# Kernel optimization log

Hardware: AMD Instinct MI355X
Metric: run time of the kernel (lower is better)

The kernel has to match this reference:

```python
import jax, jax.numpy as jnp
import numpy as np

N = 10000      # nodes
E = 320000     # edges (avg degree 32)
D_IN, D_H, D_OUT = 128, 256, 64


def setup_inputs() -> dict:
    key = jax.random.key(0)
    k0, k1, k2, k3 = jax.random.split(key, 4)
    x = jax.random.normal(k0, (N, D_IN), dtype=jnp.float32)
    edge_index = jax.random.randint(k1, (2, E), 0, N, dtype=jnp.int64)
    W1 = jax.random.normal(k2, (D_IN, D_H), dtype=jnp.float32) * 0.05
    b1 = jnp.zeros((D_H,), dtype=jnp.float32)
    W2 = jax.random.normal(k3, (D_H, D_OUT), dtype=jnp.float32) * 0.05
    b2 = jnp.zeros((D_OUT,), dtype=jnp.float32)
    return {"x": x, "edge_index": edge_index, "W1": W1, "b1": b1, "W2": W2, "b2": b2}


def gcn_conv(x, src, dst, W, b, n):
    """PyG GCNConv: linear transform, add self-loops, symmetric D^-1/2 (A+I) D^-1/2 aggregation."""
    h = x @ W                                               # [n, d_out]
    ones = jnp.ones(src.shape[0], dtype=h.dtype)
    deg = jax.ops.segment_sum(ones, dst, num_segments=n) + 1.0  # +1 for self-loop
    dinv = jax.lax.rsqrt(deg)                               # deg^{-1/2}
    norm = (dinv[src] * dinv[dst])[:, None]                 # per-edge coefficient
    agg = jax.ops.segment_sum(h[src] * norm, dst, num_segments=n)
    agg = agg + h * (1.0 / deg)[:, None]                    # self-loop: deg_i^{-1/2}*deg_i^{-1/2}
    return agg + b


def reference(x, edge_index, W1, b1, W2, b2):
    src, dst = edge_index[0], edge_index[1]
    h = jax.nn.relu(gcn_conv(x, src, dst, W1, b1, N))
    z = gcn_conv(h, src, dst, W2, b2, N)                    # [N, D_OUT]
    # decode: pairwise euclidean distance (torch.cdist p=2)
    sq = jnp.sum(z * z, axis=1)                             # [N]
    d2 = sq[:, None] + sq[None, :] - 2.0 * (z @ z.T)        # [N, N]
    d2 = jnp.maximum(d2, 0.0)
    pos = d2 > 0
    dist = jnp.where(pos, jnp.sqrt(jnp.where(pos, d2, 1.0)), 0.0)
    m = jnp.max(dist)
    m = jnp.where(m == 0, jnp.ones((), dist.dtype), m)
    return 1.0 - dist / m
```

## Files before the change

### kernel.cpp

```cpp
#include <hip/hip_runtime.h>
#include <hip/hip_bf16.h>
#include <cstdint>
#include <cstddef>

#define D_IN  128
#define D_H   256
#define D_OUT 64

typedef __attribute__((ext_vector_type(4))) float f32x4;
typedef __attribute__((ext_vector_type(8))) short s16x8;

__device__ __forceinline__ unsigned short f2bf(float f) {
  unsigned u = __float_as_uint(f);
  return (unsigned short)((u + 0x7fffu + ((u >> 16) & 1u)) >> 16);
}
__device__ __forceinline__ float bf2f(unsigned short b) {
  return __uint_as_float(((unsigned)b) << 16);
}

__global__ void prep_k(const int* __restrict__ raw, int* __restrict__ cnt,
                       int* __restrict__ cursor, int* __restrict__ gmax,
                       unsigned short* __restrict__ zb, int* __restrict__ src,
                       int* __restrict__ dst, int n, int npadElems, int E) {
  __shared__ int flag;
  if (threadIdx.x == 0) {
    int zeros = 0;
    for (int i = 0; i < 64; ++i) zeros += (raw[2 * i + 1] == 0) ? 1 : 0;
    flag = (zeros >= 60) ? 1 : 0;
  }
  __syncthreads();
  int is64 = flag;
  int T = n + 1 + npadElems + E;
  int idx = blockIdx.x * blockDim.x + threadIdx.x;
  int stride = gridDim.x * blockDim.x;
  for (; idx < T; idx += stride) {
    if (idx < n) { cnt[idx] = 0; cursor[idx] = 0; }
    else if (idx == n) gmax[0] = 0;
    else if (idx < n + 1 + npadElems) zb[(size_t)n * D_OUT + (idx - (n + 1))] = 0;
    else {
      int e = idx - (n + 1 + npadElems);
      if (is64) { src[e] = raw[2 * e]; dst[e] = raw[2 * (E + e)]; }
      else      { src[e] = raw[e];     dst[e] = raw[E + e]; }
    }
  }
}

__global__ void count_k(const int* __restrict__ dst, int* cnt, int E) {
  int idx = blockIdx.x * blockDim.x + threadIdx.x;
  int stride = gridDim.x * blockDim.x;
  for (; idx < E; idx += stride) atomicAdd(&cnt[dst[idx]], 1);
}

__global__ void scan_k(const int* __restrict__ cnt, int* __restrict__ offs,
                       float* __restrict__ dinv, int n) {
  int t = threadIdx.x;
  int lane = t & 63, wv = t >> 6;
  const int CH = 10;
  int base = t * CH;
  int local[CH];
  int s = 0;
  for (int i = 0; i < CH; ++i) {
    int v = (base + i < n) ? cnt[base + i] : 0;
    if (base + i < n) dinv[base + i] = rsqrtf((float)v + 1.0f);
    local[i] = s;
    s += v;
  }
  int sc = s;
  for (int o = 1; o < 64; o <<= 1) {
    int u = __shfl_up(sc, o, 64);
    if (lane >= o) sc += u;
  }
  __shared__ int wtot[16];
  if (lane == 63) wtot[wv] = sc;
  __syncthreads();
  if (t == 0) {
    int a = 0;
    for (int i = 0; i < 16; ++i) { int v = wtot[i]; wtot[i] = a; a += v; }
  }
  __syncthreads();
  int prefix = wtot[wv] + (sc - s);
  for (int i = 0; i < CH; ++i)
    if (base + i < n) offs[base + i] = prefix + local[i];
  if (t == 1023) offs[n] = prefix + s;
}

__global__ void fill_k(const int* __restrict__ src, const int* __restrict__ dst,
                       const int* __restrict__ offs, int* __restrict__ cursor,
                       const float* __restrict__ dinv, int* __restrict__ csr_src,
                       float* __restrict__ csr_norm, int E) {
  int idx = blockIdx.x * blockDim.x + threadIdx.x;
  int stride = gridDim.x * blockDim.x;
  for (; idx < E; idx += stride) {
    int d = dst[idx], s = src[idx];
    int pos = atomicAdd(&cursor[d], 1);
    int slot = offs[d] + pos;
    csr_src[slot] = s;
    csr_norm[slot] = dinv[s] * dinv[d];
  }
}

__global__ void gemm1_k(const float* __restrict__ A, const float* __restrict__ B,
                        unsigned short* __restrict__ C, int M, int N, int K) {
  __shared__ float As[16][64];
  __shared__ float Bs[16][64];
  int t = threadIdx.x;
  int bm = blockIdx.x * 64, bn = blockIdx.y * 64;
  int tx = t & 15, ty = t >> 4;
  int lr = t >> 2;
  int lk = (t & 3) * 4;
  int br = t >> 4;
  int bc = (t & 15) * 4;
  float acc[4][4] = {};
  for (int k0 = 0; k0 < K; k0 += 16) {
    float4 av = make_float4(0.f, 0.f, 0.f, 0.f);
    if (bm + lr < M) av = *(const float4*)&A[(size_t)(bm + lr) * K + k0 + lk];
    As[lk + 0][lr] = av.x;
    As[lk + 1][lr] = av.y;
    As[lk + 2][lr] = av.z;
    As[lk + 3][lr] = av.w;
    float4 bv = *(const float4*)&B[(size_t)(k0 + br) * N + bn + bc];
    *(float4*)&Bs[br][bc] = bv;
    __syncthreads();
#pragma unroll
    for (int k = 0; k < 16; ++k) {
      float4 a = *(const float4*)&As[k][ty * 4];
      float4 b = *(const float4*)&Bs[k][tx * 4];
      acc[0][0] += a.x * b.x; acc[0][1] += a.x * b.y; acc[0][2] += a.x * b.z; acc[0][3] += a.x * b.w;
      acc[1][0] += a.y * b.x; acc[1][1] += a.y * b.y; acc[1][2] += a.y * b.z; acc[1][3] += a.y * b.w;
      acc[2][0] += a.z * b.x; acc[2][1] += a.z * b.y; acc[2][2] += a.z * b.z; acc[2][3] += a.z * b.w;
      acc[3][0] += a.w * b.x; acc[3][1] += a.w * b.y; acc[3][2] += a.w * b.z; acc[3][3] += a.w * b.w;
    }
    __syncthreads();
  }
  for (int r = 0; r < 4; ++r) {
    int row = bm + ty * 4 + r;
    if (row < M) {
      ushort4 o;
      o.x = f2bf(acc[r][0]); o.y = f2bf(acc[r][1]);
      o.z = f2bf(acc[r][2]); o.w = f2bf(acc[r][3]);
      *(ushort4*)&C[(size_t)row * N + bn + tx * 4] = o;
    }
  }
}

__global__ void gemm2_k(const float* __restrict__ A, const float* __restrict__ B,
                        float* __restrict__ C, int M, int N, int K) {
  __shared__ float As[16][32];
  __shared__ float Bs[16][64];
  int t = threadIdx.x;
  int bm = blockIdx.x * 32;
  int tx = t & 15, ty = t >> 4;
  int lr = t >> 3;
  int lkk = (t & 7) * 2;
  int br = t >> 4;
  int bc = (t & 15) * 4;
  float acc[2][4] = {};
  for (int k0 = 0; k0 < K; k0 += 16) {
    float2 av = make_float2(0.f, 0.f);
    if (bm + lr < M) av = *(const float2*)&A[(size_t)(bm + lr) * K + k0 + lkk];
    As[lkk + 0][lr] = av.x;
    As[lkk + 1][lr] = av.y;
    float4 bv = *(const float4*)&B[(size_t)(k0 + br) * N + bc];
    *(float4*)&Bs[br][bc] = bv;
    __syncthreads();
#pragma unroll
    for (int k = 0; k < 16; ++k) {
      float a0 = As[k][ty * 2], a1 = As[k][ty * 2 + 1];
      float4 b = *(const float4*)&Bs[k][tx * 4];
      acc[0][0] += a0 * b.x; acc[0][1] += a0 * b.y; acc[0][2] += a0 * b.z; acc[0][3] += a0 * b.w;
      acc[1][0] += a1 * b.x; acc[1][1] += a1 * b.y; acc[1][2] += a1 * b.z; acc[1][3] += a1 * b.w;
    }
    __syncthreads();
  }
  for (int r = 0; r < 2; ++r) {
    int row = bm + ty * 2 + r;
    if (row < M)
      *(float4*)&C[(size_t)row * N + tx * 4] =
          make_float4(acc[r][0], acc[r][1], acc[r][2], acc[r][3]);
  }
}

__global__ void agg1_k(const unsigned short* __restrict__ hb, const int* __restrict__ offs,
                       const int* __restrict__ csr_src, const float* __restrict__ csr_norm,
                       const float* __restrict__ dinv, const float* __restrict__ b1,
                       float* __restrict__ h1, int n) {
  int wid = blockIdx.x * 4 + (threadIdx.x >> 6);
  int lane = threadIdx.x & 63;
  if (wid >= n) return;
  const ushort4* hb4 = (const ushort4*)hb;
  float di = dinv[wid];
  float selfw = di * di;
  float4 acc = *(const float4*)&b1[lane * 4];
  ushort4 sv = hb4[(size_t)wid * 64 + lane];
  acc.x += bf2f(sv.x) * selfw; acc.y += bf2f(sv.y) * selfw;
  acc.z += bf2f(sv.z) * selfw; acc.w += bf2f(sv.w) * selfw;
  int e0 = offs[wid], e1 = offs[wid + 1];
  for (int e = e0; e < e1; ++e) {
    int s = csr_src[e];
    float w = csr_norm[e];
    ushort4 v = hb4[(size_t)s * 64 + lane];
    acc.x += bf2f(v.x) * w; acc.y += bf2f(v.y) * w;
    acc.z += bf2f(v.z) * w; acc.w += bf2f(v.w) * w;
  }
  acc.x = fmaxf(acc.x, 0.f); acc.y = fmaxf(acc.y, 0.f);
  acc.z = fmaxf(acc.z, 0.f); acc.w = fmaxf(acc.w, 0.f);
  *(float4*)&h1[(size_t)wid * D_H + lane * 4] = acc;
}

__global__ void agg2_k(const float* __restrict__ h2, const int* __restrict__ offs,
                       const int* __restrict__ csr_src, const float* __restrict__ csr_norm,
                       const float* __restrict__ dinv, const float* __restrict__ b2,
                       unsigned short* __restrict__ zb, float* __restrict__ sq, int n) {
  int wid = blockIdx.x * 4 + (threadIdx.x >> 6);
  int lane = threadIdx.x & 63;
  if (wid >= n) return;
  float di = dinv[wid];
  float selfw = di * di;
  float acc = b2[lane] + h2[(size_t)wid * D_OUT + lane] * selfw;
  int e0 = offs[wid], e1 = offs[wid + 1];
  for (int e = e0; e < e1; ++e) {
    int s = csr_src[e];
    float w = csr_norm[e];
    acc += h2[(size_t)s * D_OUT + lane] * w;
  }
  unsigned short rb = f2bf(acc);
  zb[(size_t)wid * D_OUT + lane] = rb;
  float back = bf2f(rb);
  float ss = back * back;
#pragma unroll
  for (int o = 32; o > 0; o >>= 1) ss += __shfl_xor(ss, o, 64);
  if (lane == 0) sq[wid] = ss;
}

__global__ __launch_bounds__(256, 1) void decode_mfma_k(
    const unsigned short* __restrict__ zb, const float* __restrict__ sq,
    float* __restrict__ out, float* __restrict__ blockmax,
    const int* __restrict__ gmax, int n, int mode) {
  __shared__ __align__(16) char ZiB[128 * 128];
  __shared__ __align__(16) char ZjB[128 * 128];
  __shared__ float sqi[128];
  __shared__ float sqj[128];
  __shared__ float wmax[4];
  int t = threadIdx.x;

  int bi, bj;
  if (mode == 0) {
    int b = blockIdx.x;
    int tj = (int)((sqrtf(8.f * (float)b + 1.f) - 1.f) * 0.5f);
    while ((tj + 1) * (tj + 2) / 2 <= b) ++tj;
    while (tj * (tj + 1) / 2 > b) --tj;
    bj = tj;
    bi = b - tj * (tj + 1) / 2;
  } else {
    bi = blockIdx.y; bj = blockIdx.x;
  }
  int i0 = bi * 128, j0 = bj * 128;

#pragma unroll
  for (int it = 0; it < 4; ++it) {
    int c = t + it * 256;
    int row = c >> 3, s = c & 7;
    int dstb = row * 128 + ((s * 16) ^ ((row & 7) << 4));
    s16x8 vi = *(const s16x8*)&zb[(size_t)(i0 + row) * D_OUT + s * 8];
    *(s16x8*)&ZiB[dstb] = vi;
    s16x8 vj = *(const s16x8*)&zb[(size_t)(j0 + row) * D_OUT + s * 8];
    *(s16x8*)&ZjB[dstb] = vj;
  }
  if (t < 128) sqi[t] = (i0 + t < n) ? sq[i0 + t] : 0.f;
  else { int tt = t - 128; sqj[tt] = (j0 + tt < n) ? sq[j0 + tt] : 0.f; }
  __syncthreads();

  int lane = t & 63;
  int wid = t >> 6;
  int wr = (wid >> 1) * 64;
  int wc = (wid & 1) * 64;
  int lrow = lane & 15;
  int lgrp = lane >> 4;
  int swz = (lrow & 7) << 4;

  f32x4 acc[4][4] = {};
#pragma unroll
  for (int ks = 0; ks < 2; ++ks) {
    s16x8 a[4], b[4];
    int kb = (ks * 64) ^ (lgrp * 16) ^ swz;
#pragma unroll
    for (int q = 0; q < 4; ++q) {
      a[q] = *(const s16x8*)&ZiB[(wr + q * 16 + lrow) * 128 + kb];
      b[q] = *(const s16x8*)&ZjB[(wc + q * 16 + lrow) * 128 + kb];
    }
#pragma unroll
    for (int rt = 0; rt < 4; ++rt)
#pragma unroll
      for (int ct = 0; ct < 4; ++ct)
        acc[rt][ct] = __builtin_amdgcn_mfma_f32_16x16x32_bf16(a[rt], b[ct], acc[rt][ct], 0, 0, 0);
  }

  float sqa[4][4], sqb[4];
#pragma unroll
  for (int rt = 0; rt < 4; ++rt)
#pragma unroll
    for (int reg = 0; reg < 4; ++reg)
      sqa[rt][reg] = sqi[wr + rt * 16 + lgrp * 4 + reg];
#pragma unroll
  for (int ct = 0; ct < 4; ++ct) sqb[ct] = sqj[wc + ct * 16 + lrow];

  if (mode == 0) {
    float lmax = 0.f;
#pragma unroll
    for (int rt = 0; rt < 4; ++rt)
#pragma unroll
      for (int ct = 0; ct < 4; ++ct)
#pragma unroll
        for (int reg = 0; reg < 4; ++reg) {
          int i = i0 + wr + rt * 16 + lgrp * 4 + reg;
          int j = j0 + wc + ct * 16 + lrow;
          if (i < n && j < n) {
            float d2 = sqa[rt][reg] + sqb[ct] - 2.f * acc[rt][ct][reg];
            lmax = fmaxf(lmax, d2);
          }
        }
#pragma unroll
    for (int o = 32; o > 0; o >>= 1) lmax = fmaxf(lmax, __shfl_xor(lmax, o, 64));
    if (lane == 0) wmax[wid] = lmax;
    __syncthreads();
    if (t == 0) {
      float m = fmaxf(fmaxf(wmax[0], wmax[1]), fmaxf(wmax[2], wmax[3]));
      blockmax[blockIdx.x] = m;
    }
  } else {
    float m2 = __int_as_float(*gmax);
    float rsm = (m2 > 0.f) ? rsqrtf(m2) : 0.f;
#pragma unroll
    for (int rt = 0; rt < 4; ++rt)
#pragma unroll
      for (int reg = 0; reg < 4; ++reg) {
        int i = i0 + wr + rt * 16 + lgrp * 4 + reg;
        if (i >= n) continue;
        size_t rowbase = (size_t)i * n;
#pragma unroll
        for (int ct = 0; ct < 4; ++ct) {
          int j = j0 + wc + ct * 16 + lrow;
          if (j >= n) continue;
          float d2 = fmaxf(sqa[rt][reg] + sqb[ct] - 2.f * acc[rt][ct][reg], 1e-30f);
          out[rowbase + j] = 1.f - d2 * rsqrtf(d2) * rsm;
        }
      }
  }
}

__global__ void reduce_k(const float* __restrict__ bm, int* __restrict__ gmax, int nb) {
  __shared__ float s[1024];
  int t = threadIdx.x;
  float m = 0.f;
  for (int i = t; i < nb; i += 1024) m = fmaxf(m, bm[i]);
  s[t] = m;
  __syncthreads();
  for (int o = 512; o > 0; o >>= 1) {
    if (t < o) s[t] = fmaxf(s[t], s[t + o]);
    __syncthreads();
  }
  if (t == 0) gmax[0] = __float_as_int(s[0]);
}

extern "C" void kernel_launch(void* const* d_in, const int* in_sizes, int n_in,
                              void* d_out, int out_size, void* d_ws, size_t ws_size,
                              hipStream_t stream) {
  const float* x  = (const float*)d_in[0];
  const int* eraw = (const int*)d_in[1];
  const float* W1 = (const float*)d_in[2];
  const float* b1 = (const float*)d_in[3];
  const float* W2 = (const float*)d_in[4];
  const float* b2 = (const float*)d_in[5];
  float* out = (float*)d_out;

  const int n = in_sizes[0] / D_IN;
  const int E = in_sizes[1] / 2;
  const int gt = (n + 127) / 128;
  const int n_pad = gt * 128;
  const int nbU = gt * (gt + 1) / 2;

  char* p = (char*)d_ws;
  auto alloc = [&](size_t bytes) {
    void* r = (void*)p;
    p += (bytes + 255) & ~(size_t)255;
    return r;
  };
  int*   cnt      = (int*)alloc((size_t)n * 4);
  int*   offs     = (int*)alloc((size_t)(n + 1) * 4);
  int*   cursor   = (int*)alloc((size_t)n * 4);
  int*   esrc     = (int*)alloc((size_t)E * 4);
  int*   edst     = (int*)alloc((size_t)E * 4);
  int*   csr_src  = (int*)alloc((size_t)E * 4);
  float* csr_norm = (float*)alloc((size_t)E * 4);
  float* dinv     = (float*)alloc((size_t)n * 4);
  unsigned short* hb = (unsigned short*)alloc((size_t)n * D_H * 2);
  float* h1       = (float*)alloc((size_t)n * D_H * 4);
  float* h2       = (float*)alloc((size_t)n * D_OUT * 4);
  unsigned short* zbuf = (unsigned short*)alloc((size_t)n_pad * D_OUT * 2);
  float* sq       = (float*)alloc((size_t)n * 4);
  float* blockmax = (float*)alloc((size_t)nbU * 4);
  int*   gmax     = (int*)alloc(4);

  const int npadElems = (n_pad - n) * D_OUT;
  const int prepT = n + 1 + npadElems + E;
  prep_k<<<(prepT + 255) / 256, 256, 0, stream>>>(eraw, cnt, cursor, gmax, zbuf,
                                                  esrc, edst, n, npadElems, E);
  count_k<<<512, 256, 0, stream>>>(edst, cnt, E);
  scan_k<<<1, 1024, 0, stream>>>(cnt, offs, dinv, n);
  fill_k<<<512, 256, 0, stream>>>(esrc, edst, offs, cursor, dinv, csr_src, csr_norm, E);

  gemm1_k<<<dim3((n + 63) / 64, D_H / 64), 256, 0, stream>>>(x, W1, hb, n, D_H, D_IN);
  agg1_k<<<(n + 3) / 4, 256, 0, stream>>>(hb, offs, csr_src, csr_norm, dinv, b1, h1, n);

  gemm2_k<<<(n + 31) / 32, 256, 0, stream>>>(h1, W2, h2, n, D_OUT, D_H);
  agg2_k<<<(n + 3) / 4, 256, 0, stream>>>(h2, offs, csr_src, csr_norm, dinv, b2, zbuf, sq, n);

  decode_mfma_k<<<nbU, 256, 0, stream>>>(zbuf, sq, out, blockmax, gmax, n, 0);
  reduce_k<<<1, 1024, 0, stream>>>(blockmax, gmax, nbU);
  decode_mfma_k<<<dim3(gt, gt), 256, 0, stream>>>(zbuf, sq, out, blockmax, gmax, n, 1);
}
```

Baseline: 279.2 us.

## Exploit distance symmetry in decode write pass and fuse edge unpack with degree count

```diff
diff --git a/kernel.cpp b/kernel.cpp
--- a/kernel.cpp
+++ b/kernel.cpp
@@ -18,10 +18,21 @@
   return __uint_as_float(((unsigned)b) << 16);
 }
 
-__global__ void prep_k(const int* __restrict__ raw, int* __restrict__ cnt,
-                       int* __restrict__ cursor, int* __restrict__ gmax,
-                       unsigned short* __restrict__ zb, int* __restrict__ src,
-                       int* __restrict__ dst, int n, int npadElems, int E) {
+__global__ void prep_k(int* __restrict__ cnt, int* __restrict__ cursor,
+                       int* __restrict__ gmax, unsigned short* __restrict__ zb,
+                       int n, int npadElems) {
+  int T = n + 1 + npadElems;
+  int idx = blockIdx.x * blockDim.x + threadIdx.x;
+  int stride = gridDim.x * blockDim.x;
+  for (; idx < T; idx += stride) {
+    if (idx < n) { cnt[idx] = 0; cursor[idx] = 0; }
+    else if (idx == n) gmax[0] = 0;
+    else zb[(size_t)n * D_OUT + (idx - (n + 1))] = 0;
+  }
+}
+
+__global__ void countx_k(const int* __restrict__ raw, int* __restrict__ esrc,
+                         int* __restrict__ edst, int* __restrict__ cnt, int E) {
   __shared__ int flag;
   if (threadIdx.x == 0) {
     int zeros = 0;
@@ -30,25 +41,16 @@
   }
   __syncthreads();
   int is64 = flag;
-  int T = n + 1 + npadElems + E;
   int idx = blockIdx.x * blockDim.x + threadIdx.x;
   int stride = gridDim.x * blockDim.x;
-  for (; idx < T; idx += stride) {
-    if (idx < n) { cnt[idx] = 0; cursor[idx] = 0; }
-    else if (idx == n) gmax[0] = 0;
-    else if (idx < n + 1 + npadElems) zb[(size_t)n * D_OUT + (idx - (n + 1))] = 0;
-    else {
-      int e = idx - (n + 1 + npadElems);
-      if (is64) { src[e] = raw[2 * e]; dst[e] = raw[2 * (E + e)]; }
-      else      { src[e] = raw[e];     dst[e] = raw[E + e]; }
-    }
-  }
-}
-
-__global__ void count_k(const int* __restrict__ dst, int* cnt, int E) {
-  int idx = blockIdx.x * blockDim.x + threadIdx.x;
-  int stride = gridDim.x * blockDim.x;
-  for (; idx < E; idx += stride) atomicAdd(&cnt[dst[idx]], 1);
+  for (; idx < E; idx += stride) {
+    int s, d;
+    if (is64) { s = raw[2 * idx]; d = raw[2 * (E + idx)]; }
+    else      { s = raw[idx];     d = raw[E + idx]; }
+    esrc[idx] = s;
+    edst[idx] = d;
+    atomicAdd(&cnt[d], 1);
+  }
 }
 
 __global__ void scan_k(const int* __restrict__ cnt, int* __restrict__ offs,
@@ -241,19 +243,15 @@
   __shared__ float sqi[128];
   __shared__ float sqj[128];
   __shared__ float wmax[4];
+  __shared__ float LDSf[64 * 129];
   int t = threadIdx.x;
 
-  int bi, bj;
-  if (mode == 0) {
-    int b = blockIdx.x;
-    int tj = (int)((sqrtf(8.f * (float)b + 1.f) - 1.f) * 0.5f);
-    while ((tj + 1) * (tj + 2) / 2 <= b) ++tj;
-    while (tj * (tj + 1) / 2 > b) --tj;
-    bj = tj;
-    bi = b - tj * (tj + 1) / 2;
-  } else {
-    bi = blockIdx.y; bj = blockIdx.x;
-  }
+  int b = blockIdx.x;
+  int tj = (int)((sqrtf(8.f * (float)b + 1.f) - 1.f) * 0.5f);
+  while ((tj + 1) * (tj + 2) / 2 <= b) ++tj;
+  while (tj * (tj + 1) / 2 > b) --tj;
+  int bj = tj;
+  int bi = b - tj * (tj + 1) / 2;
   int i0 = bi * 128, j0 = bj * 128;
 
 #pragma unroll
@@ -281,18 +279,18 @@
   f32x4 acc[4][4] = {};
 #pragma unroll
   for (int ks = 0; ks < 2; ++ks) {
-    s16x8 a[4], b[4];
+    s16x8 a[4], bfr[4];
     int kb = (ks * 64) ^ (lgrp * 16) ^ swz;
 #pragma unroll
     for (int q = 0; q < 4; ++q) {
-      a[q] = *(const s16x8*)&ZiB[(wr + q * 16 + lrow) * 128 + kb];
-      b[q] = *(const s16x8*)&ZjB[(wc + q * 16 + lrow) * 128 + kb];
+      a[q]   = *(const s16x8*)&ZiB[(wr + q * 16 + lrow) * 128 + kb];
+      bfr[q] = *(const s16x8*)&ZjB[(wc + q * 16 + lrow) * 128 + kb];
     }
 #pragma unroll
     for (int rt = 0; rt < 4; ++rt)
 #pragma unroll
       for (int ct = 0; ct < 4; ++ct)
-        acc[rt][ct] = __builtin_amdgcn_mfma_f32_16x16x32_bf16(a[rt], b[ct], acc[rt][ct], 0, 0, 0);
+        acc[rt][ct] = __builtin_amdgcn_mfma_f32_16x16x32_bf16(a[rt], bfr[ct], acc[rt][ct], 0, 0, 0);
   }
 
   float sqa[4][4], sqb[4];
@@ -330,21 +328,45 @@
   } else {
     float m2 = __int_as_float(*gmax);
     float rsm = (m2 > 0.f) ? rsqrtf(m2) : 0.f;
-#pragma unroll
-    for (int rt = 0; rt < 4; ++rt)
-#pragma unroll
-      for (int reg = 0; reg < 4; ++reg) {
-        int i = i0 + wr + rt * 16 + lgrp * 4 + reg;
-        if (i >= n) continue;
-        size_t rowbase = (size_t)i * n;
-#pragma unroll
-        for (int ct = 0; ct < 4; ++ct) {
-          int j = j0 + wc + ct * 16 + lrow;
-          if (j >= n) continue;
-          float d2 = fmaxf(sqa[rt][reg] + sqb[ct] - 2.f * acc[rt][ct][reg], 1e-30f);
-          out[rowbase + j] = 1.f - d2 * rsqrtf(d2) * rsm;
+    bool interior = (i0 + 128 <= n) && (j0 + 128 <= n);
+    for (int h = 0; h < 2; ++h) {
+      __syncthreads();
+      if ((wid >> 1) == h) {
+#pragma unroll
+        for (int rt = 0; rt < 4; ++rt)
+#pragma unroll
+          for (int reg = 0; reg < 4; ++reg) {
+            int lr = rt * 16 + lgrp * 4 + reg;
+#pragma unroll
+            for (int ct = 0; ct < 4; ++ct) {
+              int col = wc + ct * 16 + lrow;
+              float d2 = fmaxf(sqa[rt][reg] + sqb[ct] - 2.f * acc[rt][ct][reg], 1e-30f);
+              LDSf[lr * 129 + col] = 1.f - d2 * rsqrtf(d2) * rsm;
+            }
+          }
+      }
+      __syncthreads();
+      if (interior) {
+        for (int idx = t; idx < 64 * 128; idx += 256) {
+          int r = idx >> 7, c = idx & 127;
+          out[(size_t)(i0 + h * 64 + r) * n + (j0 + c)] = LDSf[r * 129 + c];
+        }
+        for (int idx = t; idx < 128 * 64; idx += 256) {
+          int c = idx >> 6, r = idx & 63;
+          out[(size_t)(j0 + c) * n + (i0 + h * 64 + r)] = LDSf[r * 129 + c];
+        }
+      } else {
+        for (int idx = t; idx < 64 * 128; idx += 256) {
+          int r = idx >> 7, c = idx & 127;
+          int gi = i0 + h * 64 + r, gj = j0 + c;
+          if (gi < n && gj < n) {
+            float v = LDSf[r * 129 + c];
+            out[(size_t)gi * n + gj] = v;
+            out[(size_t)gj * n + gi] = v;
+          }
         }
       }
+    }
   }
 }
 
@@ -402,10 +424,9 @@
   int*   gmax     = (int*)alloc(4);
 
   const int npadElems = (n_pad - n) * D_OUT;
-  const int prepT = n + 1 + npadElems + E;
-  prep_k<<<(prepT + 255) / 256, 256, 0, stream>>>(eraw, cnt, cursor, gmax, zbuf,
-                                                  esrc, edst, n, npadElems, E);
-  count_k<<<512, 256, 0, stream>>>(edst, cnt, E);
+  prep_k<<<(n + 1 + npadElems + 255) / 256, 256, 0, stream>>>(cnt, cursor, gmax, zbuf,
+                                                              n, npadElems);
+  countx_k<<<512, 256, 0, stream>>>(eraw, esrc, edst, cnt, E);
   scan_k<<<1, 1024, 0, stream>>>(cnt, offs, dinv, n);
   fill_k<<<512, 256, 0, stream>>>(esrc, edst, offs, cursor, dinv, csr_src, csr_norm, E);
 
@@ -417,5 +438,5 @@
 
   decode_mfma_k<<<nbU, 256, 0, stream>>>(zbuf, sq, out, blockmax, gmax, n, 0);
   reduce_k<<<1, 1024, 0, stream>>>(blockmax, gmax, nbU);
-  decode_mfma_k<<<dim3(gt, gt), 256, 0, stream>>>(zbuf, sq, out, blockmax, gmax, n, 1);
-}
+  decode_mfma_k<<<nbU, 256, 0, stream>>>(zbuf, sq, out, blockmax, gmax, n, 1);
+}
```

After: 303.5 us. +8.7%, slower.
